# Kernel tuning notes

Hardware: AMD Instinct MI355X
Metric: run time of the kernel (lower is better)

The kernel has to match this reference:

```python
import jax, jax.numpy as jnp
import numpy as np

B, MAXR = 2048, 512
REQ_IN, REQ_HID, EMB1, EMB2 = 64, 256, 256, 128
INST_IN, CONCAT_HID = 64, 512


def setup_inputs() -> dict:
    key = jax.random.key(0)
    ks = jax.random.split(key, 10)
    inp = {
        "x_inst": jax.random.normal(ks[0], (B, INST_IN), dtype=jnp.float32),
        "x_req": jax.random.normal(ks[1], (B, MAXR, REQ_IN), dtype=jnp.float32),
        "x_n_req": jax.random.randint(ks[2], (B,), 0, MAXR, dtype=jnp.int32),
        # weights stored [in, out]; torch Linear has no bias for the req MLP
        "W_in": jax.random.normal(ks[3], (REQ_IN, REQ_HID), dtype=jnp.float32) / np.sqrt(REQ_IN),
        "W_e1": jax.random.normal(ks[4], (REQ_HID, EMB1), dtype=jnp.float32) / np.sqrt(REQ_HID),
        "W_e2": jax.random.normal(ks[5], (EMB1, EMB2), dtype=jnp.float32) / np.sqrt(EMB1),
        "W_c": jax.random.normal(ks[6], (INST_IN + EMB2, CONCAT_HID), dtype=jnp.float32) / np.sqrt(INST_IN + EMB2),
        "b_c": jax.random.normal(ks[7], (CONCAT_HID,), dtype=jnp.float32) * 0.01,
        "W_o": jax.random.normal(ks[8], (CONCAT_HID, 1), dtype=jnp.float32) / np.sqrt(CONCAT_HID),
        "b_o": jax.random.normal(ks[9], (1,), dtype=jnp.float32) * 0.01,
    }
    return inp


def reference(x_inst, x_req, x_n_req, W_in, W_e1, W_e2, W_c, b_c, W_o, b_o):
    act = jax.nn.relu
    # per-request MLP: [B, MAXR, REQ_IN] -> [B, MAXR, EMB1]
    h = act(jnp.einsum('bri,ih->brh', x_req, W_in))
    h = act(jnp.einsum('brh,he->bre', h, W_e1))
    # mask out padded requests (ragged lengths), then sum-pool over requests
    mask = (jnp.arange(MAXR)[None, :] < x_n_req[:, None])  # [B, MAXR]
    pooled = jnp.einsum('bre,br->be', h, mask.astype(h.dtype))  # [B, EMB1]
    req_embed = act(pooled @ W_e2)  # [B, EMB2]
    x = jnp.concatenate([x_inst, req_embed], axis=1)
    x = act(x @ W_c + b_c)
    return x @ W_o + b_o  # [B, 1]
```

## Files before the change

### kernel.cpp

```cpp
#include <hip/hip_runtime.h>


typedef __bf16 bf16x8 __attribute__((ext_vector_type(8)));
typedef __bf16 bf16x4 __attribute__((ext_vector_type(4)));
typedef float f32x4 __attribute__((ext_vector_type(4)));

#define MFMA16(a, b, c) __builtin_amdgcn_mfma_f32_16x16x32_bf16((a), (b), (c), 0, 0, 0)

#define G_BLOCKS 512

#define ASYNC_COPY16_NT(gsrc, ldst)                                   \
  __builtin_amdgcn_global_load_lds(                                   \
      (__attribute__((address_space(1))) void*)(gsrc),                \
      (__attribute__((address_space(3))) void*)(ldst), 16, 0, 2)

__global__ __launch_bounds__(256) void prep(const float* __restrict__ Win,
                                            const float* __restrict__ We1,
                                            const int* __restrict__ n_req,
                                            __bf16* __restrict__ WinT,
                                            __bf16* __restrict__ We1T,
                                            unsigned int* __restrict__ worklist,
                                            int* __restrict__ wl_count,
                                            float* __restrict__ zbuf) {
  if (blockIdx.x < 320) {
    int t = blockIdx.x * 256 + threadIdx.x;
    if (t < 16384) {
      int k = t >> 8, nn = t & 255;
      WinT[nn * 64 + k] = (__bf16)Win[t];
    } else {
      int e = t - 16384;
      int k = e >> 8, nn = e & 255;
      We1T[nn * 256 + k] = (__bf16)We1[e];
    }
    return;
  }
  ((float4*)zbuf)[threadIdx.x] = make_float4(0.f, 0.f, 0.f, 0.f);
  __shared__ int wsum[4];
  const int tid = threadIdx.x;
  const int base = tid * 8;
  int nt[8], s = 0;
#pragma unroll
  for (int j = 0; j < 8; ++j) {
    int n = n_req[base + j];
    nt[j] = (n + 63) >> 6;
    s += nt[j];
  }
  const int lane = tid & 63, wv = tid >> 6;
  int inc = s;
#pragma unroll
  for (int d = 1; d < 64; d <<= 1) {
    int u = __shfl_up(inc, d);
    if (lane >= d) inc += u;
  }
  if (lane == 63) wsum[wv] = inc;
  __syncthreads();
  int woff = 0;
  for (int w = 0; w < wv; ++w) woff += wsum[w];
  int off = woff + inc - s;
#pragma unroll
  for (int j = 0; j < 8; ++j) {
    int b = base + j;
    for (int t = 0; t < nt[j]; ++t) worklist[off++] = (unsigned int)(b * 8 + t);
  }
  if (tid == 255) wl_count[0] = woff + inc;
}

__global__ __launch_bounds__(512, 4) void mlp_pool(const float* __restrict__ x_req,
                                                   const int* __restrict__ n_req,
                                                   const __bf16* __restrict__ WinT,
                                                   const __bf16* __restrict__ We1T,
                                                   const unsigned int* __restrict__ worklist,
                                                   const int* __restrict__ wl_count,
                                                   const float* __restrict__ zbuf,
                                                   float* __restrict__ part) {
  __shared__ __align__(16) float Af[64 * 64];
  __shared__ __align__(16) __bf16 Ab[64][72];
  __shared__ __align__(16) __bf16 H[64][264];

  const int tid = threadIdx.x;
  const int wv = tid >> 6;
  const int lane = tid & 63;
  const int llo = lane & 15;
  const int lhi = lane >> 4;
  const int c0 = wv * 32;

  const int count = wl_count[0];
  int i = blockIdx.x;
  if (i >= count) return;

  bf16x8 bw1[2][2];
#pragma unroll
  for (int nf = 0; nf < 2; ++nf)
#pragma unroll
    for (int kk = 0; kk < 2; ++kk)
      bw1[nf][kk] = *(const bf16x8*)(WinT + (c0 + nf * 16 + llo) * 64 +
                                     kk * 32 + lhi * 8);

  unsigned int cit = worklist[i];
  {
    int cb = (int)(cit >> 3), ct = (int)(cit & 7);
    int cv = min(64, n_req[cb] - ct * 64);
    const float* src = x_req + ((size_t)cb * 512 + (size_t)ct * 64) * 64;
#pragma unroll
    for (int s = 0; s < 2; ++s) {
      const int row = wv * 8 + s * 4 + lhi;
      const int gc = llo ^ (row & 15);
      const float* g = (row < cv) ? (src + row * 64 + gc * 4) : (zbuf + llo * 4);
      ASYNC_COPY16_NT(g, Af + (wv * 8 + s * 4) * 64);
    }
  }

  for (; i < count; i += G_BLOCKS) {
    __syncthreads();

    {
      const int crow = wv * 8 + (lane >> 3);
      const int cc = lane & 7;
      const int r15 = crow & 15;
      f32x4 r0 = *(const f32x4*)(Af + crow * 64 + (cc ^ r15) * 4);
      f32x4 r1 = *(const f32x4*)(Af + crow * 64 + ((cc | 8) ^ r15) * 4);
      bf16x4 w0, w1;
#pragma unroll
      for (int j = 0; j < 4; ++j) {
        w0[j] = (__bf16)r0[j];
        w1[j] = (__bf16)r1[j];
      }
      *(bf16x4*)&Ab[crow][cc * 4] = w0;
      *(bf16x4*)&Ab[crow][32 + cc * 4] = w1;
    }
    __syncthreads();

    f32x4 acc[4][2];
#pragma unroll
    for (int mi = 0; mi < 4; ++mi)
#pragma unroll
      for (int nf = 0; nf < 2; ++nf) acc[mi][nf] = (f32x4){0.f, 0.f, 0.f, 0.f};
#pragma unroll
    for (int kk = 0; kk < 2; ++kk) {
      bf16x8 af[4];
#pragma unroll
      for (int mi = 0; mi < 4; ++mi)
        af[mi] = *(const bf16x8*)&Ab[mi * 16 + llo][kk * 32 + lhi * 8];
#pragma unroll
      for (int mi = 0; mi < 4; ++mi)
#pragma unroll
        for (int nf = 0; nf < 2; ++nf)
          acc[mi][nf] = MFMA16(bw1[nf][kk], af[mi], acc[mi][nf]);
    }
#pragma unroll
    for (int mi = 0; mi < 4; ++mi)
#pragma unroll
      for (int nf = 0; nf < 2; ++nf) {
        bf16x4 hv;
#pragma unroll
        for (int r = 0; r < 4; ++r) hv[r] = (__bf16)fmaxf(acc[mi][nf][r], 0.f);
        *(bf16x4*)&H[mi * 16 + llo][c0 + nf * 16 + lhi * 4] = hv;
      }
    __syncthreads();

    const int inext = i + G_BLOCKS;
    const bool hn = inext < count;
    unsigned int nit = 0u;
    if (hn) {
      nit = worklist[inext];
      int nb = (int)(nit >> 3), ntl = (int)(nit & 7);
      int nv = min(64, n_req[nb] - ntl * 64);
      const float* nsrc = x_req + ((size_t)nb * 512 + (size_t)ntl * 64) * 64;
#pragma unroll
      for (int s = 0; s < 2; ++s) {
        const int row = wv * 8 + s * 4 + lhi;
        const int gc = llo ^ (row & 15);
        const float* g = (row < nv) ? (nsrc + row * 64 + gc * 4) : (zbuf + llo * 4);
        ASYNC_COPY16_NT(g, Af + (wv * 8 + s * 4) * 64);
      }
    }

#pragma unroll
    for (int mi = 0; mi < 4; ++mi)
#pragma unroll
      for (int nf = 0; nf < 2; ++nf) acc[mi][nf] = (f32x4){0.f, 0.f, 0.f, 0.f};
#pragma unroll
    for (int kk = 0; kk < 8; ++kk) {
      bf16x8 a2[4];
#pragma unroll
      for (int mi = 0; mi < 4; ++mi)
        a2[mi] = *(const bf16x8*)&H[mi * 16 + llo][kk * 32 + lhi * 8];
#pragma unroll
      for (int nf = 0; nf < 2; ++nf) {
        bf16x8 bf_ = *(const bf16x8*)(We1T +
                        (size_t)(c0 + nf * 16 + llo) * 256 +
                        kk * 32 + lhi * 8);
#pragma unroll
        for (int mi = 0; mi < 4; ++mi)
          acc[mi][nf] = MFMA16(a2[mi], bf_, acc[mi][nf]);
      }
    }
    float colsum[2] = {0.f, 0.f};
#pragma unroll
    for (int mi = 0; mi < 4; ++mi)
#pragma unroll
      for (int nf = 0; nf < 2; ++nf)
#pragma unroll
        for (int r = 0; r < 4; ++r)
          colsum[nf] += fmaxf(acc[mi][nf][r], 0.f);

    float* outp = part + (size_t)cit * 256;
#pragma unroll
    for (int nf = 0; nf < 2; ++nf) {
      float s = colsum[nf];
      s += __shfl_xor(s, 16);
      s += __shfl_xor(s, 32);
      if (lane < 16) outp[c0 + nf * 16 + lane] = s;
    }

    cit = nit;
  }
}

__global__ __launch_bounds__(256) void head_kernel(const float* __restrict__ x_inst,
                                                   const float* __restrict__ part,
                                                   const int* __restrict__ n_req,
                                                   const float* __restrict__ We2,
                                                   const float* __restrict__ Wc,
                                                   const float* __restrict__ bc,
                                                   const float* __restrict__ Wo,
                                                   const float* __restrict__ bo,
                                                   float* __restrict__ out) {
  __shared__ float P[4][256];
  __shared__ float XC[4][192];
  __shared__ float RED[4][4];
  const int tid = threadIdx.x;
  const int r0 = blockIdx.x * 4;

  {
    int row = tid >> 6, c4 = tid & 63;
    int ntiles = (n_req[r0 + row] + 63) >> 6;
    float4 s = make_float4(0.f, 0.f, 0.f, 0.f);
    for (int tt = 0; tt < ntiles; ++tt) {
      float4 p = ((const float4*)(part + ((size_t)(r0 + row) * 8 + tt) * 256))[c4];
      s.x += p.x; s.y += p.y; s.z += p.z; s.w += p.w;
    }
    *(float4*)&P[row][c4 * 4] = s;
  }
  if (tid < 64) {
    int row = tid >> 4, c4 = tid & 15;
    float4 w = ((const float4*)(x_inst + (size_t)(r0 + row) * 64))[c4];
    *(float4*)&XC[row][c4 * 4] = w;
  }
  __syncthreads();

  {
    const int rh = tid >> 7, j = tid & 127;
    float acc[2] = {0.f, 0.f};
    for (int k4 = 0; k4 < 64; ++k4) {
      float w0 = We2[(k4 * 4 + 0) * 128 + j];
      float w1 = We2[(k4 * 4 + 1) * 128 + j];
      float w2 = We2[(k4 * 4 + 2) * 128 + j];
      float w3 = We2[(k4 * 4 + 3) * 128 + j];
#pragma unroll
      for (int rr = 0; rr < 2; ++rr) {
        float4 pv = *(const float4*)&P[rh * 2 + rr][k4 * 4];
        acc[rr] += pv.x * w0 + pv.y * w1 + pv.z * w2 + pv.w * w3;
      }
    }
#pragma unroll
    for (int rr = 0; rr < 2; ++rr)
      XC[rh * 2 + rr][64 + j] = fmaxf(acc[rr], 0.f);
  }
  __syncthreads();

  float pr[4] = {0.f, 0.f, 0.f, 0.f};
#pragma unroll
  for (int jj = 0; jj < 2; ++jj) {
    const int j = tid + jj * 256;
    float acc[4] = {0.f, 0.f, 0.f, 0.f};
    for (int k4 = 0; k4 < 48; ++k4) {
      float w0 = Wc[(k4 * 4 + 0) * 512 + j];
      float w1 = Wc[(k4 * 4 + 1) * 512 + j];
      float w2 = Wc[(k4 * 4 + 2) * 512 + j];
      float w3 = Wc[(k4 * 4 + 3) * 512 + j];
#pragma unroll
      for (int r = 0; r < 4; ++r) {
        float4 xv = *(const float4*)&XC[r][k4 * 4];
        acc[r] += xv.x * w0 + xv.y * w1 + xv.z * w2 + xv.w * w3;
      }
    }
    const float bcv = bc[j], wov = Wo[j];
#pragma unroll
    for (int r = 0; r < 4; ++r)
      pr[r] += fmaxf(acc[r] + bcv, 0.f) * wov;
  }
#pragma unroll
  for (int r = 0; r < 4; ++r) {
    pr[r] += __shfl_xor(pr[r], 1);
    pr[r] += __shfl_xor(pr[r], 2);
    pr[r] += __shfl_xor(pr[r], 4);
    pr[r] += __shfl_xor(pr[r], 8);
    pr[r] += __shfl_xor(pr[r], 16);
    pr[r] += __shfl_xor(pr[r], 32);
  }
  const int wvv = tid >> 6, lane = tid & 63;
  if (lane == 0) {
#pragma unroll
    for (int r = 0; r < 4; ++r) RED[wvv][r] = pr[r];
  }
  __syncthreads();
  if (tid < 4)
    out[r0 + tid] = RED[0][tid] + RED[1][tid] + RED[2][tid] + RED[3][tid] + bo[0];
}

extern "C" void kernel_launch(void* const* d_in, const int* in_sizes, int n_in,
                              void* d_out, int out_size, void* d_ws, size_t ws_size,
                              hipStream_t stream) {
  const float* x_inst = (const float*)d_in[0];
  const float* x_req  = (const float*)d_in[1];
  const int*   n_req  = (const int*)d_in[2];
  const float* W_in   = (const float*)d_in[3];
  const float* W_e1   = (const float*)d_in[4];
  const float* W_e2   = (const float*)d_in[5];
  const float* W_c    = (const float*)d_in[6];
  const float* b_c    = (const float*)d_in[7];
  const float* W_o    = (const float*)d_in[8];
  const float* b_o    = (const float*)d_in[9];
  float* out = (float*)d_out;

  char* ws = (char*)d_ws;
  const size_t PART_BYTES = (size_t)2048 * 8 * 256 * 4;
  float*        partbuf  = (float*)ws;
  __bf16*       WinT     = (__bf16*)(ws + PART_BYTES);
  __bf16*       We1T     = (__bf16*)(ws + PART_BYTES + (32 << 10));
  unsigned int* worklist = (unsigned int*)(ws + PART_BYTES + (160 << 10));
  int*          wl_count = (int*)(ws + PART_BYTES + (224 << 10));
  float*        zbuf     = (float*)(ws + PART_BYTES + (228 << 10));

  prep<<<321, 256, 0, stream>>>(W_in, W_e1, n_req, WinT, We1T, worklist,
                                wl_count, zbuf);
  mlp_pool<<<G_BLOCKS, 512, 0, stream>>>(x_req, n_req, WinT, We1T, worklist,
                                         wl_count, zbuf, partbuf);
  head_kernel<<<512, 256, 0, stream>>>(x_inst, partbuf, n_req, W_e2, W_c, b_c,
                                       W_o, b_o, out);
}
```

Measured before the change: 198.9 us.

## Double-buffer fp32 request tiles and convert to bf16 in registers

```diff
diff --git a/kernel.cpp b/kernel.cpp
--- a/kernel.cpp
+++ b/kernel.cpp
@@ -73,8 +73,7 @@
                                                    const int* __restrict__ wl_count,
                                                    const float* __restrict__ zbuf,
                                                    float* __restrict__ part) {
-  __shared__ __align__(16) float Af[64 * 64];
-  __shared__ __align__(16) __bf16 Ab[64][72];
+  __shared__ __align__(16) float Af[2][64 * 64];
   __shared__ __align__(16) __bf16 H[64][264];
 
   const int tid = threadIdx.x;
@@ -106,74 +105,75 @@
       const int row = wv * 8 + s * 4 + lhi;
       const int gc = llo ^ (row & 15);
       const float* g = (row < cv) ? (src + row * 64 + gc * 4) : (zbuf + llo * 4);
-      ASYNC_COPY16_NT(g, Af + (wv * 8 + s * 4) * 64);
-    }
-  }
+      ASYNC_COPY16_NT(g, &Af[0][(wv * 8 + s * 4) * 64]);
+    }
+  }
+  unsigned int nit = 0u;
+  int nv = 0;
+  if (i + G_BLOCKS < count) {
+    nit = worklist[i + G_BLOCKS];
+    int nb = (int)(nit >> 3), ntl = (int)(nit & 7);
+    nv = min(64, n_req[nb] - ntl * 64);
+  }
+  int cur = 0;
 
   for (; i < count; i += G_BLOCKS) {
     __syncthreads();
 
-    {
-      const int crow = wv * 8 + (lane >> 3);
-      const int cc = lane & 7;
-      const int r15 = crow & 15;
-      f32x4 r0 = *(const f32x4*)(Af + crow * 64 + (cc ^ r15) * 4);
-      f32x4 r1 = *(const f32x4*)(Af + crow * 64 + ((cc | 8) ^ r15) * 4);
-      bf16x4 w0, w1;
-#pragma unroll
-      for (int j = 0; j < 4; ++j) {
-        w0[j] = (__bf16)r0[j];
-        w1[j] = (__bf16)r1[j];
-      }
-      *(bf16x4*)&Ab[crow][cc * 4] = w0;
-      *(bf16x4*)&Ab[crow][32 + cc * 4] = w1;
-    }
-    __syncthreads();
-
-    f32x4 acc[4][2];
-#pragma unroll
-    for (int mi = 0; mi < 4; ++mi)
-#pragma unroll
-      for (int nf = 0; nf < 2; ++nf) acc[mi][nf] = (f32x4){0.f, 0.f, 0.f, 0.f};
-#pragma unroll
-    for (int kk = 0; kk < 2; ++kk) {
-      bf16x8 af[4];
-#pragma unroll
-      for (int mi = 0; mi < 4; ++mi)
-        af[mi] = *(const bf16x8*)&Ab[mi * 16 + llo][kk * 32 + lhi * 8];
-#pragma unroll
-      for (int mi = 0; mi < 4; ++mi)
-#pragma unroll
-        for (int nf = 0; nf < 2; ++nf)
-          acc[mi][nf] = MFMA16(bw1[nf][kk], af[mi], acc[mi][nf]);
-    }
-#pragma unroll
-    for (int mi = 0; mi < 4; ++mi)
-#pragma unroll
-      for (int nf = 0; nf < 2; ++nf) {
-        bf16x4 hv;
-#pragma unroll
-        for (int r = 0; r < 4; ++r) hv[r] = (__bf16)fmaxf(acc[mi][nf][r], 0.f);
-        *(bf16x4*)&H[mi * 16 + llo][c0 + nf * 16 + lhi * 4] = hv;
-      }
-    __syncthreads();
-
-    const int inext = i + G_BLOCKS;
-    const bool hn = inext < count;
-    unsigned int nit = 0u;
+    const bool hn = (i + G_BLOCKS) < count;
     if (hn) {
-      nit = worklist[inext];
-      int nb = (int)(nit >> 3), ntl = (int)(nit & 7);
-      int nv = min(64, n_req[nb] - ntl * 64);
-      const float* nsrc = x_req + ((size_t)nb * 512 + (size_t)ntl * 64) * 64;
+      const float* nsrc = x_req + ((size_t)(nit >> 3) * 512 + (size_t)(nit & 7) * 64) * 64;
 #pragma unroll
       for (int s = 0; s < 2; ++s) {
         const int row = wv * 8 + s * 4 + lhi;
         const int gc = llo ^ (row & 15);
         const float* g = (row < nv) ? (nsrc + row * 64 + gc * 4) : (zbuf + llo * 4);
-        ASYNC_COPY16_NT(g, Af + (wv * 8 + s * 4) * 64);
-      }
-    }
+        ASYNC_COPY16_NT(g, &Af[cur ^ 1][(wv * 8 + s * 4) * 64]);
+      }
+    }
+    unsigned int nit2 = 0u;
+    int nv2 = 0;
+    if (i + 2 * G_BLOCKS < count) {
+      nit2 = worklist[i + 2 * G_BLOCKS];
+      int nb = (int)(nit2 >> 3), ntl = (int)(nit2 & 7);
+      nv2 = min(64, n_req[nb] - ntl * 64);
+    }
+
+    const float* afb = &Af[cur][0];
+    f32x4 acc[4][2];
+#pragma unroll
+    for (int mi = 0; mi < 4; ++mi)
+#pragma unroll
+      for (int nf = 0; nf < 2; ++nf) acc[mi][nf] = (f32x4){0.f, 0.f, 0.f, 0.f};
+#pragma unroll
+    for (int kk = 0; kk < 2; ++kk)
+#pragma unroll
+      for (int mi = 0; mi < 4; ++mi) {
+        const int row = mi * 16 + llo;
+        const int cb = kk * 8 + lhi * 2;
+        f32x4 lo = *(const f32x4*)(afb + row * 64 + ((cb) ^ llo) * 4);
+        f32x4 hi = *(const f32x4*)(afb + row * 64 + ((cb + 1) ^ llo) * 4);
+        bf16x8 a;
+        a[0] = (__bf16)lo[0]; a[1] = (__bf16)lo[1];
+        a[2] = (__bf16)lo[2]; a[3] = (__bf16)lo[3];
+        a[4] = (__bf16)hi[0]; a[5] = (__bf16)hi[1];
+        a[6] = (__bf16)hi[2]; a[7] = (__bf16)hi[3];
+#pragma unroll
+        for (int nf = 0; nf < 2; ++nf)
+          acc[mi][nf] = MFMA16(bw1[nf][kk], a, acc[mi][nf]);
+      }
+#pragma unroll
+    for (int mi = 0; mi < 4; ++mi)
+#pragma unroll
+      for (int nf = 0; nf < 2; ++nf) {
+        bf16x4 hv;
+#pragma unroll
+        for (int r = 0; r < 4; ++r) hv[r] = (__bf16)fmaxf(acc[mi][nf][r], 0.f);
+        *(bf16x4*)&H[mi * 16 + llo][c0 + nf * 16 + lhi * 4] = hv;
+      }
+
+    asm volatile("s_waitcnt lgkmcnt(0)" ::: "memory");
+    __builtin_amdgcn_s_barrier();
 
 #pragma unroll
     for (int mi = 0; mi < 4; ++mi)
@@ -214,6 +214,9 @@
     }
 
     cit = nit;
+    nit = nit2;
+    nv = nv2;
+    cur ^= 1;
   }
 }
 
```

Result: faster. 190.1 us (-4.4%).
